# Performance work log

Measured on AMD Instinct MI355X. Metric: run time of the kernel, lower is better.

## Reference

```python
import jax, jax.numpy as jnp
import numpy as np

N_NODES = 50000
N_EDGES = 800000
IN_DIM = 128
HID = 128
N_POS = 100000


def setup_inputs() -> dict:
    key = jax.random.key(0)
    ks = jax.random.split(key, 16)
    inp = {
        "adj_indices": jax.random.randint(ks[0], (N_EDGES, 2), 0, N_NODES, dtype=jnp.int64)
        if jax.config.jax_enable_x64 else jax.random.randint(ks[0], (N_EDGES, 2), 0, N_NODES, dtype=jnp.int32),
        "adj_values": jax.random.uniform(ks[1], (N_EDGES,), dtype=jnp.float32),
        "num_nodes": N_NODES,
        "h": jax.random.normal(ks[2], (N_NODES, IN_DIM), dtype=jnp.float32),
        "pos_u": jax.random.randint(ks[3], (N_POS,), 0, N_NODES),
        "pos_v": jax.random.randint(ks[4], (N_POS,), 0, N_NODES),
        "neg_u": jax.random.randint(ks[5], (N_POS,), 0, N_NODES),
        "neg_v": jax.random.randint(ks[6], (N_POS,), 0, N_NODES),
    }
    # learned parameters (torch Linear: y = x @ W + b with W stored as [in, out] here)
    s1 = 1.0 / np.sqrt(IN_DIM)
    s2 = 1.0 / np.sqrt(HID)
    sd = 1.0 / np.sqrt(2 * HID)
    inp["W1"] = jax.random.uniform(ks[7], (IN_DIM, HID), minval=-s1, maxval=s1, dtype=jnp.float32)
    inp["b1"] = jax.random.uniform(ks[8], (HID,), minval=-s1, maxval=s1, dtype=jnp.float32)
    inp["W2"] = jax.random.uniform(ks[9], (HID, HID), minval=-s2, maxval=s2, dtype=jnp.float32)
    inp["b2"] = jax.random.uniform(ks[10], (HID,), minval=-s2, maxval=s2, dtype=jnp.float32)
    inp["Wd1"] = jax.random.uniform(ks[11], (2 * HID, HID), minval=-sd, maxval=sd, dtype=jnp.float32)
    inp["bd1"] = jax.random.uniform(ks[12], (HID,), minval=-sd, maxval=sd, dtype=jnp.float32)
    inp["Wd2"] = jax.random.uniform(ks[13], (HID, 1), minval=-s2, maxval=s2, dtype=jnp.float32)
    inp["bd2"] = jax.random.uniform(ks[14], (1,), minval=-s2, maxval=s2, dtype=jnp.float32)
    return inp


def reference(adj_indices, adj_values, num_nodes, h, pos_u, pos_v, neg_u, neg_v,
              W1, b1, W2, b2, Wd1, bd1, Wd2, bd2):
    row = adj_indices[:, 0]
    col = adj_indices[:, 1]
    # degree = rowwise sum of sparse values, clamped at 1
    deg = jnp.clip(jax.ops.segment_sum(adj_values, row, num_segments=num_nodes), 1.0, None)
    deg_inv = (1.0 / deg)[:, None]  # [N, 1]

    def spmm(x):  # A @ x via gather-scale-scatter over edge list
        return jax.ops.segment_sum(adj_values[:, None] * x[col], row, num_segments=num_nodes)

    h1 = jax.nn.relu((spmm(h) * deg_inv) @ W1 + b1)        # [N, HID]
    h2 = (spmm(h1) * deg_inv) @ W2 + b2                    # [N, HID]

    def decode(u, v):
        z = jnp.concatenate([h2[u], h2[v]], axis=1)        # [P, 2*HID]
        return (jax.nn.relu(z @ Wd1 + bd1) @ Wd2 + bd2)[:, 0]

    pos_scores = decode(pos_u, pos_v)
    neg_scores = decode(neg_u, neg_v)
    return pos_scores, neg_scores, h2
```

## Files before the change

### kernel.cpp

```cpp
#include <hip/hip_runtime.h>


typedef float  f32x4 __attribute__((ext_vector_type(4)));
typedef short  s16x8 __attribute__((ext_vector_type(8)));
typedef short  s16x4 __attribute__((ext_vector_type(4)));

__device__ inline short f2bf(float f){
  union { float f; unsigned u; } x; x.f = f;
  unsigned u = x.u;
  return (short)((u + 0x7FFFu + ((u >> 16) & 1u)) >> 16);
}
__device__ inline float bf2f(short h){
  union { unsigned u; float f; } c; c.u = ((unsigned)(unsigned short)h) << 16;
  return c.f;
}

__global__ void k_count(const int* __restrict__ idx, int* __restrict__ cnt,
                        int* __restrict__ rank, int E, int S){
  int i = blockIdx.x*256 + threadIdx.x;
  int e0 = i, e1 = i + S, e2 = i + 2*S, e3 = i + 3*S;
  int2 rc0, rc1, rc2, rc3;
  if (e0 < E) rc0 = ((const int2*)idx)[e0];
  if (e1 < E) rc1 = ((const int2*)idx)[e1];
  if (e2 < E) rc2 = ((const int2*)idx)[e2];
  if (e3 < E) rc3 = ((const int2*)idx)[e3];
  int r0 = 0, r1 = 0, r2 = 0, r3 = 0;
  if (e0 < E) r0 = atomicAdd(&cnt[rc0.x], 1);
  if (e1 < E) r1 = atomicAdd(&cnt[rc1.x], 1);
  if (e2 < E) r2 = atomicAdd(&cnt[rc2.x], 1);
  if (e3 < E) r3 = atomicAdd(&cnt[rc3.x], 1);
  if (e0 < E) rank[e0] = r0;
  if (e1 < E) rank[e1] = r1;
  if (e2 < E) rank[e2] = r2;
  if (e3 < E) rank[e3] = r3;
}

__global__ void k_blocksum(const int* __restrict__ rp, int* __restrict__ bsum, int N){
  int i = blockIdx.x*256 + threadIdx.x;
  int c = (i < N) ? rp[i] : 0;
  #pragma unroll
  for (int off = 1; off < 64; off <<= 1) c += __shfl_xor(c, off);
  __shared__ int s[4];
  if ((threadIdx.x & 63) == 0) s[threadIdx.x >> 6] = c;
  __syncthreads();
  if (threadIdx.x == 0) bsum[blockIdx.x] = s[0] + s[1] + s[2] + s[3];
}

__global__ void k_scanb(const int* __restrict__ bsum, int* __restrict__ boff,
                        int* __restrict__ rpN, int B){
  __shared__ int s[256];
  int t = threadIdx.x;
  int run = 0;
  for (int base = 0; base < B; base += 256){
    int c = (base + t < B) ? bsum[base + t] : 0;
    s[t] = c;
    __syncthreads();
    #pragma unroll
    for (int off = 1; off < 256; off <<= 1){
      int v = s[t];
      int u = (t >= off) ? s[t-off] : 0;
      __syncthreads();
      s[t] = v + u;
      __syncthreads();
    }
    if (base + t < B) boff[base + t] = run + s[t] - c;
    run += s[255];
    __syncthreads();
  }
  if (t == 0) rpN[0] = run;
}

__global__ void k_addoff(int* __restrict__ rp, const int* __restrict__ boff, int N){
  __shared__ int s[256];
  int t = threadIdx.x;
  int i = blockIdx.x*256 + t;
  int c = (i < N) ? rp[i] : 0;
  s[t] = c;
  __syncthreads();
  #pragma unroll
  for (int off = 1; off < 256; off <<= 1){
    int v = s[t];
    int u = (t >= off) ? s[t-off] : 0;
    __syncthreads();
    s[t] = v + u;
    __syncthreads();
  }
  if (i < N) rp[i] = s[t] - c + boff[blockIdx.x];
}

__global__ void k_scatter(const int* __restrict__ idx, const float* __restrict__ vals,
                          const int* __restrict__ rp, const int* __restrict__ rank,
                          int2* __restrict__ ce, int E, int S){
  int i = blockIdx.x*256 + threadIdx.x;
  #pragma unroll
  for (int q = 0; q < 4; ++q){
    int e = i + q*S;
    if (e < E){
      int2 rc = ((const int2*)idx)[e];
      int p = rp[rc.x] + rank[e];
      ce[p] = make_int2(rc.y, __float_as_int(vals[e]));
    }
  }
}

__global__ void k_prep(const float* __restrict__ h, const float* __restrict__ W1,
                       const float* __restrict__ W2, const float* __restrict__ Wd1,
                       short* __restrict__ hb, short* __restrict__ Wh,
                       short* __restrict__ Wl, short* __restrict__ WdP, int n4){
  int gid = blockIdx.x*256 + threadIdx.x;
  if (gid < n4){
    float4 v = ((const float4*)h)[gid];
    s16x4 o; o[0]=f2bf(v.x); o[1]=f2bf(v.y); o[2]=f2bf(v.z); o[3]=f2bf(v.w);
    *(s16x4*)&hb[(size_t)gid*4] = o;
  } else if (gid < n4 + 32768){
    int idx = gid - n4;
    int b = idx & 7, lane = (idx >> 3) & 63, kk = (idx >> 9) & 3, j = (idx >> 11) & 7;
    int m = idx >> 14;
    const float* W = m ? W2 : W1;
    int row = kk*32 + 8*(lane >> 4) + b;
    int col = j*16 + (lane & 15);
    float x = W[row*128 + col];
    short hbit = f2bf(x);
    Wh[idx] = hbit;
    Wl[idx] = f2bf(x - bf2f(hbit));
  } else if (gid < n4 + 65536){
    int idx = gid - n4 - 32768;
    int b = idx & 7, lane = (idx >> 3) & 63, kk = (idx >> 9) & 7, j = (idx >> 12) & 7;
    int row = kk*32 + 8*(lane >> 4) + b;
    int col = j*16 + (lane & 15);
    WdP[idx] = f2bf(Wd1[row*128 + col]);
  }
}

__global__ void k_spmm(const int* __restrict__ rp, const int2* __restrict__ ce,
                       const short* __restrict__ Xb, float* __restrict__ out, int N){
  int r = blockIdx.x*16 + (threadIdx.x >> 4);
  int t = threadIdx.x & 15;
  if (r >= N) return;
  f32x4 a0 = {0.f,0.f,0.f,0.f}, a1 = {0.f,0.f,0.f,0.f};
  float vs0 = 0.f, vs1 = 0.f;
  int e0 = rp[r], e1 = rp[r+1];
  int e = e0;
  for (; e + 3 < e1; e += 4){
    int2 p0 = ce[e], p1 = ce[e+1], p2 = ce[e+2], p3 = ce[e+3];
    s16x8 x0 = *(const s16x8*)&Xb[(size_t)p0.x*128 + t*8];
    s16x8 x1 = *(const s16x8*)&Xb[(size_t)p1.x*128 + t*8];
    s16x8 x2 = *(const s16x8*)&Xb[(size_t)p2.x*128 + t*8];
    s16x8 x3 = *(const s16x8*)&Xb[(size_t)p3.x*128 + t*8];
    float v0 = __int_as_float(p0.y), v1 = __int_as_float(p1.y);
    float v2 = __int_as_float(p2.y), v3 = __int_as_float(p3.y);
    #pragma unroll
    for (int b = 0; b < 4; ++b){
      a0[b] = fmaf(v0, bf2f(x0[b]), a0[b]);   a1[b] = fmaf(v0, bf2f(x0[b+4]), a1[b]);
      a0[b] = fmaf(v1, bf2f(x1[b]), a0[b]);   a1[b] = fmaf(v1, bf2f(x1[b+4]), a1[b]);
      a0[b] = fmaf(v2, bf2f(x2[b]), a0[b]);   a1[b] = fmaf(v2, bf2f(x2[b+4]), a1[b]);
      a0[b] = fmaf(v3, bf2f(x3[b]), a0[b]);   a1[b] = fmaf(v3, bf2f(x3[b+4]), a1[b]);
    }
    vs0 += v0 + v2; vs1 += v1 + v3;
  }
  for (; e < e1; ++e){
    int2 p0 = ce[e];
    s16x8 x0 = *(const s16x8*)&Xb[(size_t)p0.x*128 + t*8];
    float v0 = __int_as_float(p0.y);
    #pragma unroll
    for (int b = 0; b < 4; ++b){
      a0[b] = fmaf(v0, bf2f(x0[b]), a0[b]);
      a1[b] = fmaf(v0, bf2f(x0[b+4]), a1[b]);
    }
    vs0 += v0;
  }
  float di = 1.0f / fmaxf(vs0 + vs1, 1.0f);
  a0 *= di; a1 *= di;
  *(f32x4*)&out[(size_t)r*128 + t*8]     = a0;
  *(f32x4*)&out[(size_t)r*128 + t*8 + 4] = a1;
}

template<bool RELU, bool EMIT_F32, bool EMIT_BF16>
__global__ __launch_bounds__(256)
void k_mgemm(const float* __restrict__ A, const short* __restrict__ Wh,
             const short* __restrict__ Wl, const float* __restrict__ bias,
             float* __restrict__ out, short* __restrict__ out_bf, int M)
{
  const int wave = threadIdx.x >> 6;
  const int lane = threadIdx.x & 63;
  const int l15 = lane & 15, lg = lane >> 4;
  const int wrow = blockIdx.x*64 + wave*16;
  int arow = wrow + l15; if (arow >= M) arow = M - 1;

  s16x8 ah[4], al[4];
  #pragma unroll
  for (int kk = 0; kk < 4; ++kk){
    const float* src = &A[(size_t)arow*128 + kk*32 + 8*lg];
    float4 x0 = *(const float4*)src;
    float4 x1 = *(const float4*)(src + 4);
    float xs[8] = {x0.x,x0.y,x0.z,x0.w,x1.x,x1.y,x1.z,x1.w};
    #pragma unroll
    for (int b = 0; b < 8; ++b){
      short hb = f2bf(xs[b]);
      ah[kk][b] = hb;
      al[kk][b] = f2bf(xs[b] - bf2f(hb));
    }
  }

  const s16x8* WH = (const s16x8*)Wh;
  const s16x8* WL = (const s16x8*)Wl;
  f32x4 acc[8];
  #pragma unroll
  for (int j = 0; j < 8; ++j) acc[j] = (f32x4){0.f,0.f,0.f,0.f};

  #pragma unroll
  for (int j = 0; j < 8; ++j){
    #pragma unroll
    for (int kk = 0; kk < 4; ++kk){
      s16x8 bh = WH[(j*4 + kk)*64 + lane];
      s16x8 bl = WL[(j*4 + kk)*64 + lane];
      acc[j] = __builtin_amdgcn_mfma_f32_16x16x32_bf16(ah[kk], bh, acc[j], 0, 0, 0);
      acc[j] = __builtin_amdgcn_mfma_f32_16x16x32_bf16(al[kk], bh, acc[j], 0, 0, 0);
      acc[j] = __builtin_amdgcn_mfma_f32_16x16x32_bf16(ah[kk], bl, acc[j], 0, 0, 0);
    }
  }

  #pragma unroll
  for (int j = 0; j < 8; ++j){
    int col = j*16 + l15;
    float bb = bias[col];
    #pragma unroll
    for (int r = 0; r < 4; ++r){
      int row = wrow + 4*lg + r;
      if (row < M){
        float v = acc[j][r] + bb;
        if (RELU) v = fmaxf(v, 0.f);
        if (EMIT_F32)  out[(size_t)row*128 + col] = v;
        if (EMIT_BF16) out_bf[(size_t)row*128 + col] = f2bf(v);
      }
    }
  }
}

__global__ __launch_bounds__(256)
void k_decode(const short* __restrict__ h2b, const short* __restrict__ WdP,
              const float* __restrict__ bd1, const float* __restrict__ wd2,
              const float* __restrict__ bd2,
              const int* __restrict__ pos_u, const int* __restrict__ pos_v,
              const int* __restrict__ neg_u, const int* __restrict__ neg_v,
              float* __restrict__ out_pos, float* __restrict__ out_neg, int P)
{
  __shared__ short Bs[32768];

  const int which = blockIdx.y;
  const int* iu = which ? neg_u : pos_u;
  const int* iv = which ? neg_v : pos_v;
  float* out = which ? out_neg : out_pos;

  const int wave = threadIdx.x >> 6;
  const int lane = threadIdx.x & 63;
  const int l15 = lane & 15, lg = lane >> 4;
  const int wbase = blockIdx.x*128 + wave*32;

  int ra0 = wbase + l15;      if (ra0 >= P) ra0 = P - 1;
  int ra1 = wbase + 16 + l15; if (ra1 >= P) ra1 = P - 1;
  int u0 = iu[ra0], v0 = iv[ra0];
  int u1 = iu[ra1], v1 = iv[ra1];

  s16x8 a0[8], a1[8];
  #pragma unroll
  for (int kk = 0; kk < 8; ++kk){
    int kg = kk*32 + 8*lg;
    const short* s0 = (kg < 128) ? h2b + (size_t)u0*128 + kg
                                 : h2b + (size_t)v0*128 + (kg - 128);
    const short* s1 = (kg < 128) ? h2b + (size_t)u1*128 + kg
                                 : h2b + (size_t)v1*128 + (kg - 128);
    a0[kk] = *(const s16x8*)s0;
    a1[kk] = *(const s16x8*)s1;
  }

  {
    const int4* src = (const int4*)WdP;
    int4* dst = (int4*)Bs;
    #pragma unroll
    for (int i = 0; i < 16; ++i)
      dst[threadIdx.x + i*256] = src[threadIdx.x + i*256];
  }
  __syncthreads();

  const s16x8* Wp = (const s16x8*)Bs;
  f32x4 acc0[8], acc1[8];
  #pragma unroll
  for (int j = 0; j < 8; ++j){
    acc0[j] = (f32x4){0.f,0.f,0.f,0.f};
    acc1[j] = (f32x4){0.f,0.f,0.f,0.f};
  }

  #pragma unroll
  for (int j = 0; j < 8; ++j){
    #pragma unroll
    for (int kk = 0; kk < 8; ++kk){
      s16x8 b = Wp[(j*8 + kk)*64 + lane];
      acc0[j] = __builtin_amdgcn_mfma_f32_16x16x32_bf16(a0[kk], b, acc0[j], 0, 0, 0);
      acc1[j] = __builtin_amdgcn_mfma_f32_16x16x32_bf16(a1[kk], b, acc1[j], 0, 0, 0);
    }
  }

  float part0[4] = {0,0,0,0}, part1[4] = {0,0,0,0};
  #pragma unroll
  for (int j = 0; j < 8; ++j){
    int col = j*16 + l15;
    float bb = bd1[col], ww = wd2[col];
    #pragma unroll
    for (int r = 0; r < 4; ++r){
      part0[r] = fmaf(fmaxf(acc0[j][r] + bb, 0.f), ww, part0[r]);
      part1[r] = fmaf(fmaxf(acc1[j][r] + bb, 0.f), ww, part1[r]);
    }
  }
  #pragma unroll
  for (int off = 1; off < 16; off <<= 1){
    #pragma unroll
    for (int r = 0; r < 4; ++r){
      part0[r] += __shfl_xor(part0[r], off);
      part1[r] += __shfl_xor(part1[r], off);
    }
  }
  if (l15 == 0){
    float b2v = bd2[0];
    int m0 = wbase + 4*lg, m1 = wbase + 16 + 4*lg;
    #pragma unroll
    for (int r = 0; r < 4; ++r){
      if (m0 + r < P) out[m0 + r] = part0[r] + b2v;
      if (m1 + r < P) out[m1 + r] = part1[r] + b2v;
    }
  }
}

extern "C" void kernel_launch(void* const* d_in, const int* in_sizes, int n_in,
                              void* d_out, int out_size, void* d_ws, size_t ws_size,
                              hipStream_t stream){
  const int*   adj   = (const int*)  d_in[0];
  const float* av    = (const float*)d_in[1];
  const float* h     = (const float*)d_in[3];
  const int*   pos_u = (const int*)  d_in[4];
  const int*   pos_v = (const int*)  d_in[5];
  const int*   neg_u = (const int*)  d_in[6];
  const int*   neg_v = (const int*)  d_in[7];
  const float* W1    = (const float*)d_in[8];
  const float* b1    = (const float*)d_in[9];
  const float* W2    = (const float*)d_in[10];
  const float* b2    = (const float*)d_in[11];
  const float* Wd1   = (const float*)d_in[12];
  const float* bd1   = (const float*)d_in[13];
  const float* Wd2   = (const float*)d_in[14];
  const float* bd2   = (const float*)d_in[15];

  const int E = in_sizes[0] / 2;
  const int N = in_sizes[3] / 128;
  const int P = in_sizes[4];
  const int NB = (N + 255) / 256;
  const int n4 = N * 128 / 4;

  auto al = [](size_t x){ return (x + 255) & ~(size_t)255; };
  char* base = (char*)d_ws;
  size_t off = 0;
  int*   rp     = (int*)(base + off);   off = al(off + (size_t)(N+1)*4);
  int*   rank   = (int*)(base + off);   off = al(off + (size_t)E*4);
  int*   bsum   = (int*)(base + off);   off = al(off + (size_t)NB*4);
  int*   boff   = (int*)(base + off);   off = al(off + (size_t)NB*4);
  int2*  ce     = (int2*)(base + off);  off = al(off + (size_t)E*8);
  short* W12h   = (short*)(base + off); off = al(off + (size_t)32768*2);
  short* W12l   = (short*)(base + off); off = al(off + (size_t)32768*2);
  short* WdP    = (short*)(base + off); off = al(off + (size_t)32768*2);
  short* hb     = (short*)(base + off); off = al(off + (size_t)N*128*2);
  short* h1b    = (short*)(base + off); off = al(off + (size_t)N*128*2);
  short* h2b    = (short*)(base + off); off = al(off + (size_t)N*128*2);

  float* scores_pos = (float*)d_out;
  float* scores_neg = scores_pos + P;
  float* h2         = scores_neg + P;

  hipMemsetAsync(rp, 0, (size_t)(N+1)*4, stream);

  const int EG = ((E + 3) / 4 + 255) / 256;
  const int S  = EG * 256;
  k_count   <<<EG, 256, 0, stream>>>(adj, rp, rank, E, S);
  k_blocksum<<<NB, 256, 0, stream>>>(rp, bsum, N);
  k_scanb   <<<1, 256, 0, stream>>>(bsum, boff, rp + N, NB);
  k_addoff  <<<NB, 256, 0, stream>>>(rp, boff, N);
  k_scatter <<<EG, 256, 0, stream>>>(adj, av, rp, rank, ce, E, S);
  k_prep    <<<(n4 + 65536 + 255)/256, 256, 0, stream>>>(h, W1, W2, Wd1, hb, W12h, W12l, WdP, n4);

  k_spmm<<<(N+15)/16, 256, 0, stream>>>(rp, ce, hb, h2, N);
  k_mgemm<true , false, true ><<<(N+63)/64, 256, 0, stream>>>(h2, W12h, W12l, b1, nullptr, h1b, N);

  k_spmm<<<(N+15)/16, 256, 0, stream>>>(rp, ce, h1b, h2, N);
  k_mgemm<false, true , true ><<<(N+63)/64, 256, 0, stream>>>(h2, W12h + 16384, W12l + 16384, b2, h2, h2b, N);

  dim3 dgrid((P+127)/128, 2);
  k_decode<<<dgrid, 256, 0, stream>>>(h2b, WdP, bd1, Wd2, bd2,
                                      pos_u, pos_v, neg_u, neg_v,
                                      scores_pos, scores_neg, P);
}
```

Baseline: 308.6 us.

## Fuse SpMM into GEMM per layer and merge scan, scatter and prep launches

New measurement: 295.5 us. 1.04x faster.

```diff
diff --git a/kernel.cpp b/kernel.cpp
--- a/kernel.cpp
+++ b/kernel.cpp
@@ -46,34 +46,34 @@
   if (threadIdx.x == 0) bsum[blockIdx.x] = s[0] + s[1] + s[2] + s[3];
 }
 
-__global__ void k_scanb(const int* __restrict__ bsum, int* __restrict__ boff,
-                        int* __restrict__ rpN, int B){
+__global__ void k_addoff(int* __restrict__ rp, const int* __restrict__ bsum,
+                         int NB, int N){
   __shared__ int s[256];
-  int t = threadIdx.x;
-  int run = 0;
-  for (int base = 0; base < B; base += 256){
-    int c = (base + t < B) ? bsum[base + t] : 0;
-    s[t] = c;
-    __syncthreads();
-    #pragma unroll
-    for (int off = 1; off < 256; off <<= 1){
-      int v = s[t];
-      int u = (t >= off) ? s[t-off] : 0;
-      __syncthreads();
-      s[t] = v + u;
-      __syncthreads();
-    }
-    if (base + t < B) boff[base + t] = run + s[t] - c;
-    run += s[255];
-    __syncthreads();
-  }
-  if (t == 0) rpN[0] = run;
-}
-
-__global__ void k_addoff(int* __restrict__ rp, const int* __restrict__ boff, int N){
-  __shared__ int s[256];
-  int t = threadIdx.x;
-  int i = blockIdx.x*256 + t;
+  __shared__ int pre_s, tot_s;
+  const int t = threadIdx.x;
+  const int bid = blockIdx.x;
+
+  int pre = 0, tot = 0;
+  for (int j = t; j < NB; j += 256){
+    int b = bsum[j];
+    tot += b;
+    if (j < bid) pre += b;
+  }
+  #pragma unroll
+  for (int off = 1; off < 64; off <<= 1){
+    pre += __shfl_xor(pre, off);
+    tot += __shfl_xor(tot, off);
+  }
+  __shared__ int ps[4], ts[4];
+  if ((t & 63) == 0){ ps[t >> 6] = pre; ts[t >> 6] = tot; }
+  __syncthreads();
+  if (t == 0){
+    pre_s = ps[0] + ps[1] + ps[2] + ps[3];
+    tot_s = ts[0] + ts[1] + ts[2] + ts[3];
+  }
+  __syncthreads();
+
+  int i = bid*256 + t;
   int c = (i < N) ? rp[i] : 0;
   s[t] = c;
   __syncthreads();
@@ -85,120 +85,132 @@
     s[t] = v + u;
     __syncthreads();
   }
-  if (i < N) rp[i] = s[t] - c + boff[blockIdx.x];
-}
-
-__global__ void k_scatter(const int* __restrict__ idx, const float* __restrict__ vals,
-                          const int* __restrict__ rp, const int* __restrict__ rank,
-                          int2* __restrict__ ce, int E, int S){
-  int i = blockIdx.x*256 + threadIdx.x;
-  #pragma unroll
-  for (int q = 0; q < 4; ++q){
-    int e = i + q*S;
-    if (e < E){
-      int2 rc = ((const int2*)idx)[e];
-      int p = rp[rc.x] + rank[e];
-      ce[p] = make_int2(rc.y, __float_as_int(vals[e]));
-    }
-  }
-}
-
-__global__ void k_prep(const float* __restrict__ h, const float* __restrict__ W1,
-                       const float* __restrict__ W2, const float* __restrict__ Wd1,
-                       short* __restrict__ hb, short* __restrict__ Wh,
-                       short* __restrict__ Wl, short* __restrict__ WdP, int n4){
-  int gid = blockIdx.x*256 + threadIdx.x;
+  if (i < N) rp[i] = s[t] - c + pre_s;
+  if (bid == NB-1 && t == 0) rp[N] = tot_s;
+}
+
+__global__ void k_sp(const int* __restrict__ idx, const float* __restrict__ vals,
+                     const int* __restrict__ rp, const int* __restrict__ rank,
+                     int2* __restrict__ ce, int E, int S, int EG,
+                     const float* __restrict__ h, const float* __restrict__ W1,
+                     const float* __restrict__ W2, const float* __restrict__ Wd1,
+                     short* __restrict__ hb, short* __restrict__ Wh,
+                     short* __restrict__ Wl, short* __restrict__ WdP, int n4){
+  int bid = blockIdx.x;
+  if (bid < EG){
+    int i = bid*256 + threadIdx.x;
+    #pragma unroll
+    for (int q = 0; q < 4; ++q){
+      int e = i + q*S;
+      if (e < E){
+        int2 rc = ((const int2*)idx)[e];
+        int p = rp[rc.x] + rank[e];
+        ce[p] = make_int2(rc.y, __float_as_int(vals[e]));
+      }
+    }
+    return;
+  }
+  int gid = (bid - EG)*256 + threadIdx.x;
   if (gid < n4){
     float4 v = ((const float4*)h)[gid];
     s16x4 o; o[0]=f2bf(v.x); o[1]=f2bf(v.y); o[2]=f2bf(v.z); o[3]=f2bf(v.w);
     *(s16x4*)&hb[(size_t)gid*4] = o;
   } else if (gid < n4 + 32768){
-    int idx = gid - n4;
-    int b = idx & 7, lane = (idx >> 3) & 63, kk = (idx >> 9) & 3, j = (idx >> 11) & 7;
-    int m = idx >> 14;
+    int idx2 = gid - n4;
+    int b = idx2 & 7, lane = (idx2 >> 3) & 63, kk = (idx2 >> 9) & 3, j = (idx2 >> 11) & 7;
+    int m = idx2 >> 14;
     const float* W = m ? W2 : W1;
     int row = kk*32 + 8*(lane >> 4) + b;
     int col = j*16 + (lane & 15);
     float x = W[row*128 + col];
     short hbit = f2bf(x);
-    Wh[idx] = hbit;
-    Wl[idx] = f2bf(x - bf2f(hbit));
+    Wh[idx2] = hbit;
+    Wl[idx2] = f2bf(x - bf2f(hbit));
   } else if (gid < n4 + 65536){
-    int idx = gid - n4 - 32768;
-    int b = idx & 7, lane = (idx >> 3) & 63, kk = (idx >> 9) & 7, j = (idx >> 12) & 7;
+    int idx2 = gid - n4 - 32768;
+    int b = idx2 & 7, lane = (idx2 >> 3) & 63, kk = (idx2 >> 9) & 7, j = (idx2 >> 12) & 7;
     int row = kk*32 + 8*(lane >> 4) + b;
     int col = j*16 + (lane & 15);
-    WdP[idx] = f2bf(Wd1[row*128 + col]);
-  }
-}
-
-__global__ void k_spmm(const int* __restrict__ rp, const int2* __restrict__ ce,
-                       const short* __restrict__ Xb, float* __restrict__ out, int N){
-  int r = blockIdx.x*16 + (threadIdx.x >> 4);
-  int t = threadIdx.x & 15;
-  if (r >= N) return;
-  f32x4 a0 = {0.f,0.f,0.f,0.f}, a1 = {0.f,0.f,0.f,0.f};
-  float vs0 = 0.f, vs1 = 0.f;
-  int e0 = rp[r], e1 = rp[r+1];
-  int e = e0;
-  for (; e + 3 < e1; e += 4){
-    int2 p0 = ce[e], p1 = ce[e+1], p2 = ce[e+2], p3 = ce[e+3];
-    s16x8 x0 = *(const s16x8*)&Xb[(size_t)p0.x*128 + t*8];
-    s16x8 x1 = *(const s16x8*)&Xb[(size_t)p1.x*128 + t*8];
-    s16x8 x2 = *(const s16x8*)&Xb[(size_t)p2.x*128 + t*8];
-    s16x8 x3 = *(const s16x8*)&Xb[(size_t)p3.x*128 + t*8];
-    float v0 = __int_as_float(p0.y), v1 = __int_as_float(p1.y);
-    float v2 = __int_as_float(p2.y), v3 = __int_as_float(p3.y);
-    #pragma unroll
-    for (int b = 0; b < 4; ++b){
-      a0[b] = fmaf(v0, bf2f(x0[b]), a0[b]);   a1[b] = fmaf(v0, bf2f(x0[b+4]), a1[b]);
-      a0[b] = fmaf(v1, bf2f(x1[b]), a0[b]);   a1[b] = fmaf(v1, bf2f(x1[b+4]), a1[b]);
-      a0[b] = fmaf(v2, bf2f(x2[b]), a0[b]);   a1[b] = fmaf(v2, bf2f(x2[b+4]), a1[b]);
-      a0[b] = fmaf(v3, bf2f(x3[b]), a0[b]);   a1[b] = fmaf(v3, bf2f(x3[b+4]), a1[b]);
-    }
-    vs0 += v0 + v2; vs1 += v1 + v3;
-  }
-  for (; e < e1; ++e){
-    int2 p0 = ce[e];
-    s16x8 x0 = *(const s16x8*)&Xb[(size_t)p0.x*128 + t*8];
-    float v0 = __int_as_float(p0.y);
-    #pragma unroll
-    for (int b = 0; b < 4; ++b){
-      a0[b] = fmaf(v0, bf2f(x0[b]), a0[b]);
-      a1[b] = fmaf(v0, bf2f(x0[b+4]), a1[b]);
-    }
-    vs0 += v0;
-  }
-  float di = 1.0f / fmaxf(vs0 + vs1, 1.0f);
-  a0 *= di; a1 *= di;
-  *(f32x4*)&out[(size_t)r*128 + t*8]     = a0;
-  *(f32x4*)&out[(size_t)r*128 + t*8 + 4] = a1;
+    WdP[idx2] = f2bf(Wd1[row*128 + col]);
+  }
 }
 
 template<bool RELU, bool EMIT_F32, bool EMIT_BF16>
 __global__ __launch_bounds__(256)
-void k_mgemm(const float* __restrict__ A, const short* __restrict__ Wh,
+void k_layer(const int* __restrict__ rp, const int2* __restrict__ ce,
+             const short* __restrict__ Xb, const short* __restrict__ Wh,
              const short* __restrict__ Wl, const float* __restrict__ bias,
-             float* __restrict__ out, short* __restrict__ out_bf, int M)
+             float* __restrict__ outf, short* __restrict__ outb, int N)
 {
-  const int wave = threadIdx.x >> 6;
-  const int lane = threadIdx.x & 63;
+  __shared__ float As[64][132];
+  const int tid = threadIdx.x;
+  const int brow = blockIdx.x*64;
+
+  {
+    const int t = tid & 15;
+    const int rloc = tid >> 4;
+    for (int g = 0; g < 4; ++g){
+      int lrow = g*16 + rloc;
+      int row = brow + lrow;
+      f32x4 a0 = {0.f,0.f,0.f,0.f}, a1 = {0.f,0.f,0.f,0.f};
+      float vs0 = 0.f, vs1 = 0.f;
+      if (row < N){
+        int e0 = rp[row], e1 = rp[row+1];
+        int e = e0;
+        for (; e + 3 < e1; e += 4){
+          int2 p0 = ce[e], p1 = ce[e+1], p2 = ce[e+2], p3 = ce[e+3];
+          s16x8 x0 = *(const s16x8*)&Xb[(size_t)p0.x*128 + t*8];
+          s16x8 x1 = *(const s16x8*)&Xb[(size_t)p1.x*128 + t*8];
+          s16x8 x2 = *(const s16x8*)&Xb[(size_t)p2.x*128 + t*8];
+          s16x8 x3 = *(const s16x8*)&Xb[(size_t)p3.x*128 + t*8];
+          float v0 = __int_as_float(p0.y), v1 = __int_as_float(p1.y);
+          float v2 = __int_as_float(p2.y), v3 = __int_as_float(p3.y);
+          #pragma unroll
+          for (int b = 0; b < 4; ++b){
+            a0[b] = fmaf(v0, bf2f(x0[b]), a0[b]);   a1[b] = fmaf(v0, bf2f(x0[b+4]), a1[b]);
+            a0[b] = fmaf(v1, bf2f(x1[b]), a0[b]);   a1[b] = fmaf(v1, bf2f(x1[b+4]), a1[b]);
+            a0[b] = fmaf(v2, bf2f(x2[b]), a0[b]);   a1[b] = fmaf(v2, bf2f(x2[b+4]), a1[b]);
+            a0[b] = fmaf(v3, bf2f(x3[b]), a0[b]);   a1[b] = fmaf(v3, bf2f(x3[b+4]), a1[b]);
+          }
+          vs0 += v0 + v2; vs1 += v1 + v3;
+        }
+        for (; e < e1; ++e){
+          int2 p0 = ce[e];
+          s16x8 x0 = *(const s16x8*)&Xb[(size_t)p0.x*128 + t*8];
+          float v0 = __int_as_float(p0.y);
+          #pragma unroll
+          for (int b = 0; b < 4; ++b){
+            a0[b] = fmaf(v0, bf2f(x0[b]), a0[b]);
+            a1[b] = fmaf(v0, bf2f(x0[b+4]), a1[b]);
+          }
+          vs0 += v0;
+        }
+        float di = 1.0f / fmaxf(vs0 + vs1, 1.0f);
+        a0 *= di; a1 *= di;
+      }
+      *(f32x4*)&As[lrow][t*8]     = a0;
+      *(f32x4*)&As[lrow][t*8 + 4] = a1;
+    }
+  }
+  __syncthreads();
+
+  const int wave = tid >> 6;
+  const int lane = tid & 63;
   const int l15 = lane & 15, lg = lane >> 4;
-  const int wrow = blockIdx.x*64 + wave*16;
-  int arow = wrow + l15; if (arow >= M) arow = M - 1;
+  const int arow = wave*16 + l15;
 
   s16x8 ah[4], al[4];
   #pragma unroll
   for (int kk = 0; kk < 4; ++kk){
-    const float* src = &A[(size_t)arow*128 + kk*32 + 8*lg];
+    const float* src = &As[arow][kk*32 + 8*lg];
     float4 x0 = *(const float4*)src;
     float4 x1 = *(const float4*)(src + 4);
     float xs[8] = {x0.x,x0.y,x0.z,x0.w,x1.x,x1.y,x1.z,x1.w};
     #pragma unroll
     for (int b = 0; b < 8; ++b){
-      short hb = f2bf(xs[b]);
-      ah[kk][b] = hb;
-      al[kk][b] = f2bf(xs[b] - bf2f(hb));
+      short hb2 = f2bf(xs[b]);
+      ah[kk][b] = hb2;
+      al[kk][b] = f2bf(xs[b] - bf2f(hb2));
     }
   }
 
@@ -226,12 +238,12 @@
     float bb = bias[col];
     #pragma unroll
     for (int r = 0; r < 4; ++r){
-      int row = wrow + 4*lg + r;
-      if (row < M){
+      int row = brow + wave*16 + 4*lg + r;
+      if (row < N){
         float v = acc[j][r] + bb;
         if (RELU) v = fmaxf(v, 0.f);
-        if (EMIT_F32)  out[(size_t)row*128 + col] = v;
-        if (EMIT_BF16) out_bf[(size_t)row*128 + col] = f2bf(v);
+        if (EMIT_F32)  outf[(size_t)row*128 + col] = v;
+        if (EMIT_BF16) outb[(size_t)row*128 + col] = f2bf(v);
       }
     }
   }
@@ -362,7 +374,6 @@
   int*   rp     = (int*)(base + off);   off = al(off + (size_t)(N+1)*4);
   int*   rank   = (int*)(base + off);   off = al(off + (size_t)E*4);
   int*   bsum   = (int*)(base + off);   off = al(off + (size_t)NB*4);
-  int*   boff   = (int*)(base + off);   off = al(off + (size_t)NB*4);
   int2*  ce     = (int2*)(base + off);  off = al(off + (size_t)E*8);
   short* W12h   = (short*)(base + off); off = al(off + (size_t)32768*2);
   short* W12l   = (short*)(base + off); off = al(off + (size_t)32768*2);
@@ -379,18 +390,18 @@
 
   const int EG = ((E + 3) / 4 + 255) / 256;
   const int S  = EG * 256;
+  const int PB = (n4 + 65536 + 255) / 256;
   k_count   <<<EG, 256, 0, stream>>>(adj, rp, rank, E, S);
   k_blocksum<<<NB, 256, 0, stream>>>(rp, bsum, N);
-  k_scanb   <<<1, 256, 0, stream>>>(bsum, boff, rp + N, NB);
-  k_addoff  <<<NB, 256, 0, stream>>>(rp, boff, N);
-  k_scatter <<<EG, 256, 0, stream>>>(adj, av, rp, rank, ce, E, S);
-  k_prep    <<<(n4 + 65536 + 255)/256, 256, 0, stream>>>(h, W1, W2, Wd1, hb, W12h, W12l, WdP, n4);
-
-  k_spmm<<<(N+15)/16, 256, 0, stream>>>(rp, ce, hb, h2, N);
-  k_mgemm<true , false, true ><<<(N+63)/64, 256, 0, stream>>>(h2, W12h, W12l, b1, nullptr, h1b, N);
-
-  k_spmm<<<(N+15)/16, 256, 0, stream>>>(rp, ce, h1b, h2, N);
-  k_mgemm<false, true , true ><<<(N+63)/64, 256, 0, stream>>>(h2, W12h + 16384, W12l + 16384, b2, h2, h2b, N);
+  k_addoff  <<<NB, 256, 0, stream>>>(rp, bsum, NB, N);
+  k_sp      <<<EG + PB, 256, 0, stream>>>(adj, av, rp, rank, ce, E, S, EG,
+                                          h, W1, W2, Wd1, hb, W12h, W12l, WdP, n4);
+
+  k_layer<true , false, true ><<<(N+63)/64, 256, 0, stream>>>(
+      rp, ce, hb, W12h, W12l, b1, nullptr, h1b, N);
+
+  k_layer<false, true , true ><<<(N+63)/64, 256, 0, stream>>>(
+      rp, ce, h1b, W12h + 16384, W12l + 16384, b2, h2, h2b, N);
 
   dim3 dgrid((P+127)/128, 2);
   k_decode<<<dgrid, 256, 0, stream>>>(h2b, WdP, bd1, Wd2, bd2,
```
